# Optimization experiments

Hardware: AMD Instinct MI355X
Metric: run time of the kernel (lower is better)

## Reference

```python
import jax, jax.numpy as jnp
import numpy as np

EPS = 1e-12

def l2_normalize(x):
    # matches torch: x * rsqrt(max(sum(x^2), eps))
    ss = jnp.sum(x * x, axis=-1, keepdims=True)
    return x * jax.lax.rsqrt(jnp.maximum(ss, EPS))

B, S, D = 256, 197, 768          # batch, tokens, embed_dim (ViT-B)
H, LEN, KS, POOL = 12, 5, 17, 50  # heads, prompt length, conv kernel, pool_size
DUAL_LEN = 2 * (LEN + KS - 1)     # 42
PD = D + (KS - 1) * H             # 960


def setup_inputs() -> dict:
    key = jax.random.key(0)
    ks = jax.random.split(key, 8)
    x_embed = jax.random.normal(ks[0], (B, S, D), jnp.float32)
    # learned params
    prompt = jax.random.uniform(ks[1], (1, DUAL_LEN, PD), jnp.float32, -1.0, 1.0)
    prompt_key = jax.random.uniform(ks[2], (POOL, D // 4), jnp.float32, -1.0, 1.0)
    W1 = jax.random.normal(ks[3], (D // 2, D), jnp.float32) * (1.0 / np.sqrt(D))
    b1 = jnp.zeros((D // 2,), jnp.float32)
    W2 = jax.random.normal(ks[4], (D // 4, D // 2), jnp.float32) * (1.0 / np.sqrt(D // 2))
    b2 = jnp.zeros((D // 4,), jnp.float32)
    return {"x_embed": x_embed, "prompt": prompt, "prompt_key": prompt_key,
            "W1": W1, "b1": b1, "W2": W2, "b2": b2, "layer_num": 0}


def reference(x_embed, prompt, prompt_key, W1, b1, W2, b2, layer_num):
    # embedding_key == 'mean'
    x_mean = jnp.mean(x_embed, axis=1)                       # [B, D]
    # prompt_embed_matcher: Linear(D, D/2) -> ReLU -> Linear(D/2, D/4)
    h = jax.nn.relu(x_mean @ W1.T + b1)                      # [B, D/2]
    feat = h @ W2.T + b2                                     # [B, D/4]
    # cosine similarity against key pool (eval path: full pool)
    key_norm = l2_normalize(prompt_key)                      # [POOL, D/4]
    x_norm = l2_normalize(feat)                              # [B, D/4]
    similarity = x_norm @ key_norm.T                         # [B, POOL] == (K @ X^T)^T
    # prefix-tune prompt: repeat over batch and split into (dual, len, heads, head_dim)
    p = prompt[layer_num]                                    # [DUAL_LEN, PD]
    Ltot, E = p.shape
    batched_prompt = jnp.broadcast_to(p, (x_embed.shape[0], Ltot, E))
    batched_prompt = batched_prompt.reshape(x_embed.shape[0], 2, Ltot // 2, H, E // H)
    return similarity, x_norm, batched_prompt
```

## Files before the change

kernel.cpp:

```cpp
#include <hip/hip_runtime.h>

#define NB 256
#define NS 197
#define ND 768
#define ND2 384
#define ND4 192
#define NPOOL 50
#define PROMPT_FLOATS 40320
#define PROMPT_V4 10080
#define TB 2

__global__ __launch_bounds__(768) void k_mean_bcast(
    const float* __restrict__ x,
    const float* __restrict__ prompt,
    const int* __restrict__ layer_num,
    float* __restrict__ xmean,
    float* __restrict__ out_prompt)
{
    const int b = blockIdx.x;
    const int tid = threadIdx.x;
    const int lane = tid % 192;
    const int g = tid / 192;

    const float4* __restrict__ xr =
        reinterpret_cast<const float4*>(x) + (size_t)b * (NS * (ND / 4));
    float4 acc = make_float4(0.f, 0.f, 0.f, 0.f);
    for (int s = g; s < NS; s += 4) {
        float4 v = xr[s * (ND / 4) + lane];
        acc.x += v.x; acc.y += v.y; acc.z += v.z; acc.w += v.w;
    }
    __shared__ float4 part[4][192];
    part[g][lane] = acc;
    __syncthreads();
    if (g == 0) {
        float4 p0 = part[0][lane], p1 = part[1][lane];
        float4 p2 = part[2][lane], p3 = part[3][lane];
        const float inv = 1.0f / (float)NS;
        float4 m;
        m.x = (p0.x + p1.x + p2.x + p3.x) * inv;
        m.y = (p0.y + p1.y + p2.y + p3.y) * inv;
        m.z = (p0.z + p1.z + p2.z + p3.z) * inv;
        m.w = (p0.w + p1.w + p2.w + p3.w) * inv;
        reinterpret_cast<float4*>(xmean + (size_t)b * ND)[lane] = m;
    }

    const float4* __restrict__ pv =
        reinterpret_cast<const float4*>(prompt + (size_t)layer_num[0] * PROMPT_FLOATS);
    float4* __restrict__ ov =
        reinterpret_cast<float4*>(out_prompt) + (size_t)b * PROMPT_V4;
    for (int i = tid; i < PROMPT_V4; i += 768) {
        ov[i] = pv[i];
    }
}

__global__ __launch_bounds__(512) void k_mlp(
    const float* __restrict__ xmean,
    const float* __restrict__ W1,
    const float* __restrict__ b1,
    const float* __restrict__ W2,
    const float* __restrict__ b2,
    const float* __restrict__ key,
    float* __restrict__ sim,
    float* __restrict__ xnorm)
{
    const int tid = threadIdx.x;
    const int g   = tid >> 4;
    const int l   = tid & 15;
    const int b0  = blockIdx.x * TB;

    __shared__ __align__(16) float xm[TB][ND];
    __shared__ __align__(16) float hs[TB][ND2];
    __shared__ __align__(16) float fs[TB][ND4];
    __shared__ float rs[TB];

    {
        const float4* __restrict__ src =
            reinterpret_cast<const float4*>(xmean + (size_t)b0 * ND);
        float4* dst = reinterpret_cast<float4*>(&xm[0][0]);
        for (int i = tid; i < TB * ND / 4; i += 512) dst[i] = src[i];
    }
    __syncthreads();

    {
        const float4* __restrict__ x0v = reinterpret_cast<const float4*>(&xm[0][0]);
        const float4* __restrict__ x1v = reinterpret_cast<const float4*>(&xm[1][0]);
        for (int r = 0; r < ND2 / 32; ++r) {
            const int i = g + 32 * r;
            const float4* __restrict__ w =
                reinterpret_cast<const float4*>(W1 + (size_t)i * ND);
            float a0 = 0.f, a1 = 0.f;
            #pragma unroll
            for (int s = 0; s < ND / 64; ++s) {
                float4 wv = w[s * 16 + l];
                float4 x0 = x0v[s * 16 + l];
                float4 x1 = x1v[s * 16 + l];
                a0 += wv.x * x0.x + wv.y * x0.y + wv.z * x0.z + wv.w * x0.w;
                a1 += wv.x * x1.x + wv.y * x1.y + wv.z * x1.z + wv.w * x1.w;
            }
            #pragma unroll
            for (int m = 8; m; m >>= 1) {
                a0 += __shfl_xor(a0, m);
                a1 += __shfl_xor(a1, m);
            }
            if (l == 0) {
                float bias = b1[i];
                hs[0][i] = fmaxf(a0 + bias, 0.f);
                hs[1][i] = fmaxf(a1 + bias, 0.f);
            }
        }
    }
    __syncthreads();

    {
        const float4* __restrict__ h0v = reinterpret_cast<const float4*>(&hs[0][0]);
        const float4* __restrict__ h1v = reinterpret_cast<const float4*>(&hs[1][0]);
        for (int r = 0; r < ND4 / 32; ++r) {
            const int j = g + 32 * r;
            const float4* __restrict__ w =
                reinterpret_cast<const float4*>(W2 + (size_t)j * ND2);
            float a0 = 0.f, a1 = 0.f;
            #pragma unroll
            for (int s = 0; s < ND2 / 64; ++s) {
                float4 wv = w[s * 16 + l];
                float4 h0 = h0v[s * 16 + l];
                float4 h1 = h1v[s * 16 + l];
                a0 += wv.x * h0.x + wv.y * h0.y + wv.z * h0.z + wv.w * h0.w;
                a1 += wv.x * h1.x + wv.y * h1.y + wv.z * h1.z + wv.w * h1.w;
            }
            #pragma unroll
            for (int m = 8; m; m >>= 1) {
                a0 += __shfl_xor(a0, m);
                a1 += __shfl_xor(a1, m);
            }
            if (l == 0) {
                float bias = b2[j];
                fs[0][j] = a0 + bias;
                fs[1][j] = a1 + bias;
            }
        }
    }
    __syncthreads();

    if (tid < TB * 64) {
        const int w = tid >> 6, ll = tid & 63;
        float v0 = fs[w][ll], v1 = fs[w][ll + 64], v2 = fs[w][ll + 128];
        float ss = v0 * v0 + v1 * v1 + v2 * v2;
        #pragma unroll
        for (int m = 32; m; m >>= 1) ss += __shfl_xor(ss, m);
        if (ll == 0) rs[w] = rsqrtf(fmaxf(ss, 1e-12f));
    }
    __syncthreads();

    for (int i = tid; i < TB * ND4; i += 512) {
        const int b = i / ND4, j = i - b * ND4;
        float v = fs[b][j] * rs[b];
        fs[b][j] = v;
        xnorm[(size_t)(b0 + b) * ND4 + j] = v;
    }
    __syncthreads();

    {
        const float4* __restrict__ x0v = reinterpret_cast<const float4*>(&fs[0][0]);
        const float4* __restrict__ x1v = reinterpret_cast<const float4*>(&fs[1][0]);
        for (int p = g; p < NPOOL; p += 32) {
            const float4* __restrict__ kr =
                reinterpret_cast<const float4*>(key + (size_t)p * ND4);
            float kk = 0.f, d0 = 0.f, d1 = 0.f;
            #pragma unroll
            for (int s = 0; s < ND4 / 64; ++s) {
                float4 kv = kr[s * 16 + l];
                float4 x0 = x0v[s * 16 + l];
                float4 x1 = x1v[s * 16 + l];
                kk += kv.x * kv.x + kv.y * kv.y + kv.z * kv.z + kv.w * kv.w;
                d0 += kv.x * x0.x + kv.y * x0.y + kv.z * x0.z + kv.w * x0.w;
                d1 += kv.x * x1.x + kv.y * x1.y + kv.z * x1.z + kv.w * x1.w;
            }
            #pragma unroll
            for (int m = 8; m; m >>= 1) {
                kk += __shfl_xor(kk, m);
                d0 += __shfl_xor(d0, m);
                d1 += __shfl_xor(d1, m);
            }
            if (l == 0) {
                float krs = rsqrtf(fmaxf(kk, 1e-12f));
                sim[(size_t)(b0 + 0) * NPOOL + p] = d0 * krs;
                sim[(size_t)(b0 + 1) * NPOOL + p] = d1 * krs;
            }
        }
    }
}

extern "C" void kernel_launch(void* const* d_in, const int* in_sizes, int n_in,
                              void* d_out, int out_size, void* d_ws, size_t ws_size,
                              hipStream_t stream) {
    const float* x        = (const float*)d_in[0];
    const float* prompt   = (const float*)d_in[1];
    const float* key      = (const float*)d_in[2];
    const float* W1       = (const float*)d_in[3];
    const float* b1       = (const float*)d_in[4];
    const float* W2       = (const float*)d_in[5];
    const float* b2       = (const float*)d_in[6];
    const int*   layer_nm = (const int*)d_in[7];

    float* out        = (float*)d_out;
    float* sim        = out;
    float* xnorm      = out + 12800;
    float* out_prompt = out + 12800 + 49152;

    float* xmean = (float*)d_ws;

    hipLaunchKernelGGL(k_mean_bcast, dim3(NB), dim3(768), 0, stream,
                       x, prompt, layer_nm, xmean, out_prompt);
    hipLaunchKernelGGL(k_mlp, dim3(NB / TB), dim3(512), 0, stream,
                       xmean, W1, b1, W2, b2, key, sim, xnorm);
}
```

Baseline: 327.0 us.

## Fuse mean, MLP, similarity and prompt broadcast into one per-batch kernel

Merges the mean/broadcast kernel and the MLP/similarity kernel into a single kernel with one 768-thread block per batch row. The token mean stays in shared memory and feeds the MLP directly, so the workspace round trip and the second launch go away. In exchange, each block now streams the full W1/W2 weights for one row instead of sharing them across two rows, which doubles weight reads, though these likely hit in L2. The prompt broadcast writes are moved to the end of the block.

Result: faster. 266.1 us (-18.6%).

```diff
diff --git a/kernel.cpp b/kernel.cpp
--- a/kernel.cpp
+++ b/kernel.cpp
@@ -8,184 +8,144 @@
 #define NPOOL 50
 #define PROMPT_FLOATS 40320
 #define PROMPT_V4 10080
-#define TB 2
 
-__global__ __launch_bounds__(768) void k_mean_bcast(
+__global__ __launch_bounds__(768) void k_fused(
     const float* __restrict__ x,
     const float* __restrict__ prompt,
     const int* __restrict__ layer_num,
-    float* __restrict__ xmean,
-    float* __restrict__ out_prompt)
-{
-    const int b = blockIdx.x;
-    const int tid = threadIdx.x;
-    const int lane = tid % 192;
-    const int g = tid / 192;
-
-    const float4* __restrict__ xr =
-        reinterpret_cast<const float4*>(x) + (size_t)b * (NS * (ND / 4));
-    float4 acc = make_float4(0.f, 0.f, 0.f, 0.f);
-    for (int s = g; s < NS; s += 4) {
-        float4 v = xr[s * (ND / 4) + lane];
-        acc.x += v.x; acc.y += v.y; acc.z += v.z; acc.w += v.w;
-    }
-    __shared__ float4 part[4][192];
-    part[g][lane] = acc;
-    __syncthreads();
-    if (g == 0) {
-        float4 p0 = part[0][lane], p1 = part[1][lane];
-        float4 p2 = part[2][lane], p3 = part[3][lane];
-        const float inv = 1.0f / (float)NS;
-        float4 m;
-        m.x = (p0.x + p1.x + p2.x + p3.x) * inv;
-        m.y = (p0.y + p1.y + p2.y + p3.y) * inv;
-        m.z = (p0.z + p1.z + p2.z + p3.z) * inv;
-        m.w = (p0.w + p1.w + p2.w + p3.w) * inv;
-        reinterpret_cast<float4*>(xmean + (size_t)b * ND)[lane] = m;
-    }
-
-    const float4* __restrict__ pv =
-        reinterpret_cast<const float4*>(prompt + (size_t)layer_num[0] * PROMPT_FLOATS);
-    float4* __restrict__ ov =
-        reinterpret_cast<float4*>(out_prompt) + (size_t)b * PROMPT_V4;
-    for (int i = tid; i < PROMPT_V4; i += 768) {
-        ov[i] = pv[i];
-    }
-}
-
-__global__ __launch_bounds__(512) void k_mlp(
-    const float* __restrict__ xmean,
     const float* __restrict__ W1,
     const float* __restrict__ b1,
     const float* __restrict__ W2,
     const float* __restrict__ b2,
     const float* __restrict__ key,
     float* __restrict__ sim,
-    float* __restrict__ xnorm)
+    float* __restrict__ xnorm,
+    float* __restrict__ out_prompt)
 {
+    const int b   = blockIdx.x;
     const int tid = threadIdx.x;
     const int g   = tid >> 4;
     const int l   = tid & 15;
-    const int b0  = blockIdx.x * TB;
 
-    __shared__ __align__(16) float xm[TB][ND];
-    __shared__ __align__(16) float hs[TB][ND2];
-    __shared__ __align__(16) float fs[TB][ND4];
-    __shared__ float rs[TB];
+    __shared__ __align__(16) float4 part[4][192];
+    __shared__ __align__(16) float xm[ND];
+    __shared__ __align__(16) float hs[ND2];
+    __shared__ __align__(16) float fs[ND4];
+    __shared__ float rsv;
 
     {
-        const float4* __restrict__ src =
-            reinterpret_cast<const float4*>(xmean + (size_t)b0 * ND);
-        float4* dst = reinterpret_cast<float4*>(&xm[0][0]);
-        for (int i = tid; i < TB * ND / 4; i += 512) dst[i] = src[i];
-    }
-    __syncthreads();
-
-    {
-        const float4* __restrict__ x0v = reinterpret_cast<const float4*>(&xm[0][0]);
-        const float4* __restrict__ x1v = reinterpret_cast<const float4*>(&xm[1][0]);
-        for (int r = 0; r < ND2 / 32; ++r) {
-            const int i = g + 32 * r;
-            const float4* __restrict__ w =
-                reinterpret_cast<const float4*>(W1 + (size_t)i * ND);
-            float a0 = 0.f, a1 = 0.f;
-            #pragma unroll
-            for (int s = 0; s < ND / 64; ++s) {
-                float4 wv = w[s * 16 + l];
-                float4 x0 = x0v[s * 16 + l];
-                float4 x1 = x1v[s * 16 + l];
-                a0 += wv.x * x0.x + wv.y * x0.y + wv.z * x0.z + wv.w * x0.w;
-                a1 += wv.x * x1.x + wv.y * x1.y + wv.z * x1.z + wv.w * x1.w;
-            }
-            #pragma unroll
-            for (int m = 8; m; m >>= 1) {
-                a0 += __shfl_xor(a0, m);
-                a1 += __shfl_xor(a1, m);
-            }
-            if (l == 0) {
-                float bias = b1[i];
-                hs[0][i] = fmaxf(a0 + bias, 0.f);
-                hs[1][i] = fmaxf(a1 + bias, 0.f);
-            }
+        const int lane = tid % 192;
+        const int sg   = tid / 192;
+        const float4* __restrict__ xr =
+            reinterpret_cast<const float4*>(x) + (size_t)b * (NS * (ND / 4));
+        float4 acc = make_float4(0.f, 0.f, 0.f, 0.f);
+        for (int s = sg; s < NS; s += 4) {
+            float4 v = xr[s * (ND / 4) + lane];
+            acc.x += v.x; acc.y += v.y; acc.z += v.z; acc.w += v.w;
+        }
+        part[sg][lane] = acc;
+        __syncthreads();
+        if (sg == 0) {
+            float4 p0 = part[0][lane], p1 = part[1][lane];
+            float4 p2 = part[2][lane], p3 = part[3][lane];
+            const float inv = 1.0f / (float)NS;
+            float4 m;
+            m.x = (p0.x + p1.x + p2.x + p3.x) * inv;
+            m.y = (p0.y + p1.y + p2.y + p3.y) * inv;
+            m.z = (p0.z + p1.z + p2.z + p3.z) * inv;
+            m.w = (p0.w + p1.w + p2.w + p3.w) * inv;
+            reinterpret_cast<float4*>(xm)[lane] = m;
         }
     }
     __syncthreads();
 
     {
-        const float4* __restrict__ h0v = reinterpret_cast<const float4*>(&hs[0][0]);
-        const float4* __restrict__ h1v = reinterpret_cast<const float4*>(&hs[1][0]);
-        for (int r = 0; r < ND4 / 32; ++r) {
-            const int j = g + 32 * r;
+        const float4* __restrict__ xv = reinterpret_cast<const float4*>(xm);
+        #pragma unroll
+        for (int r = 0; r < ND2 / 48; ++r) {
+            const int i = g + 48 * r;
             const float4* __restrict__ w =
-                reinterpret_cast<const float4*>(W2 + (size_t)j * ND2);
-            float a0 = 0.f, a1 = 0.f;
+                reinterpret_cast<const float4*>(W1 + (size_t)i * ND);
+            float a = 0.f;
             #pragma unroll
-            for (int s = 0; s < ND2 / 64; ++s) {
+            for (int s = 0; s < ND / 64; ++s) {
                 float4 wv = w[s * 16 + l];
-                float4 h0 = h0v[s * 16 + l];
-                float4 h1 = h1v[s * 16 + l];
-                a0 += wv.x * h0.x + wv.y * h0.y + wv.z * h0.z + wv.w * h0.w;
-                a1 += wv.x * h1.x + wv.y * h1.y + wv.z * h1.z + wv.w * h1.w;
+                float4 xv4 = xv[s * 16 + l];
+                a += wv.x * xv4.x + wv.y * xv4.y + wv.z * xv4.z + wv.w * xv4.w;
             }
             #pragma unroll
-            for (int m = 8; m; m >>= 1) {
-                a0 += __shfl_xor(a0, m);
-                a1 += __shfl_xor(a1, m);
-            }
-            if (l == 0) {
-                float bias = b2[j];
-                fs[0][j] = a0 + bias;
-                fs[1][j] = a1 + bias;
-            }
+            for (int m = 8; m; m >>= 1) a += __shfl_xor(a, m);
+            if (l == 0) hs[i] = fmaxf(a + b1[i], 0.f);
         }
     }
     __syncthreads();
 
-    if (tid < TB * 64) {
-        const int w = tid >> 6, ll = tid & 63;
-        float v0 = fs[w][ll], v1 = fs[w][ll + 64], v2 = fs[w][ll + 128];
+    {
+        const float4* __restrict__ hv = reinterpret_cast<const float4*>(hs);
+        #pragma unroll
+        for (int r = 0; r < ND4 / 48; ++r) {
+            const int j = g + 48 * r;
+            const float4* __restrict__ w =
+                reinterpret_cast<const float4*>(W2 + (size_t)j * ND2);
+            float a = 0.f;
+            #pragma unroll
+            for (int s = 0; s < ND2 / 64; ++s) {
+                float4 wv = w[s * 16 + l];
+                float4 hv4 = hv[s * 16 + l];
+                a += wv.x * hv4.x + wv.y * hv4.y + wv.z * hv4.z + wv.w * hv4.w;
+            }
+            #pragma unroll
+            for (int m = 8; m; m >>= 1) a += __shfl_xor(a, m);
+            if (l == 0) fs[j] = a + b2[j];
+        }
+    }
+    __syncthreads();
+
+    if (tid < 64) {
+        float v0 = fs[tid], v1 = fs[tid + 64], v2 = fs[tid + 128];
         float ss = v0 * v0 + v1 * v1 + v2 * v2;
         #pragma unroll
         for (int m = 32; m; m >>= 1) ss += __shfl_xor(ss, m);
-        if (ll == 0) rs[w] = rsqrtf(fmaxf(ss, 1e-12f));
+        if (tid == 0) rsv = rsqrtf(fmaxf(ss, 1e-12f));
     }
     __syncthreads();
 
-    for (int i = tid; i < TB * ND4; i += 512) {
-        const int b = i / ND4, j = i - b * ND4;
-        float v = fs[b][j] * rs[b];
-        fs[b][j] = v;
-        xnorm[(size_t)(b0 + b) * ND4 + j] = v;
+    if (tid < ND4) {
+        float v = fs[tid] * rsv;
+        fs[tid] = v;
+        xnorm[(size_t)b * ND4 + tid] = v;
     }
     __syncthreads();
 
     {
-        const float4* __restrict__ x0v = reinterpret_cast<const float4*>(&fs[0][0]);
-        const float4* __restrict__ x1v = reinterpret_cast<const float4*>(&fs[1][0]);
-        for (int p = g; p < NPOOL; p += 32) {
+        const float4* __restrict__ xv = reinterpret_cast<const float4*>(fs);
+        for (int p = g; p < NPOOL; p += 48) {
             const float4* __restrict__ kr =
                 reinterpret_cast<const float4*>(key + (size_t)p * ND4);
-            float kk = 0.f, d0 = 0.f, d1 = 0.f;
+            float kk = 0.f, d = 0.f;
             #pragma unroll
             for (int s = 0; s < ND4 / 64; ++s) {
                 float4 kv = kr[s * 16 + l];
-                float4 x0 = x0v[s * 16 + l];
-                float4 x1 = x1v[s * 16 + l];
+                float4 xv4 = xv[s * 16 + l];
                 kk += kv.x * kv.x + kv.y * kv.y + kv.z * kv.z + kv.w * kv.w;
-                d0 += kv.x * x0.x + kv.y * x0.y + kv.z * x0.z + kv.w * x0.w;
-                d1 += kv.x * x1.x + kv.y * x1.y + kv.z * x1.z + kv.w * x1.w;
+                d  += kv.x * xv4.x + kv.y * xv4.y + kv.z * xv4.z + kv.w * xv4.w;
             }
             #pragma unroll
             for (int m = 8; m; m >>= 1) {
                 kk += __shfl_xor(kk, m);
-                d0 += __shfl_xor(d0, m);
-                d1 += __shfl_xor(d1, m);
+                d  += __shfl_xor(d, m);
             }
-            if (l == 0) {
-                float krs = rsqrtf(fmaxf(kk, 1e-12f));
-                sim[(size_t)(b0 + 0) * NPOOL + p] = d0 * krs;
-                sim[(size_t)(b0 + 1) * NPOOL + p] = d1 * krs;
-            }
+            if (l == 0) sim[(size_t)b * NPOOL + p] = d * rsqrtf(fmaxf(kk, 1e-12f));
+        }
+    }
+
+    {
+        const float4* __restrict__ pv =
+            reinterpret_cast<const float4*>(prompt + (size_t)layer_num[0] * PROMPT_FLOATS);
+        float4* __restrict__ ov =
+            reinterpret_cast<float4*>(out_prompt) + (size_t)b * PROMPT_V4;
+        for (int i = tid; i < PROMPT_V4; i += 768) {
+            ov[i] = pv[i];
         }
     }
 }
@@ -207,10 +167,7 @@
     float* xnorm      = out + 12800;
     float* out_prompt = out + 12800 + 49152;
 
-    float* xmean = (float*)d_ws;
-
-    hipLaunchKernelGGL(k_mean_bcast, dim3(NB), dim3(768), 0, stream,
-                       x, prompt, layer_nm, xmean, out_prompt);
-    hipLaunchKernelGGL(k_mlp, dim3(NB / TB), dim3(512), 0, stream,
-                       xmean, W1, b1, W2, b2, key, sim, xnorm);
+    hipLaunchKernelGGL(k_fused, dim3(NB), dim3(768), 0, stream,
+                       x, prompt, layer_nm, W1, b1, W2, b2, key,
+                       sim, xnorm, out_prompt);
 }
```

## Split token-mean into per-chunk partial sums and batch four rows per MLP block

Applied to the files above, without the earlier changes.

The mean reduction now runs as 2048 blocks, each summing a 25-row chunk of one batch element and copying a slice of the prompt broadcast. Partial sums go to workspace and are combined in the MLP kernel's prologue, which removes the shared-memory combine step. The MLP kernel now handles four batch rows per block instead of two, so each W1/W2/key load is reused across more rows. In exchange it writes more intermediate data, and the MLP stage runs on only 64 blocks.

New measurement: 281.9 us. -13.8%, faster.

```diff
diff --git a/kernel.cpp b/kernel.cpp
--- a/kernel.cpp
+++ b/kernel.cpp
@@ -3,58 +3,52 @@
 #define NB 256
 #define NS 197
 #define ND 768
+#define NDV4 192
 #define ND2 384
 #define ND4 192
 #define NPOOL 50
 #define PROMPT_FLOATS 40320
 #define PROMPT_V4 10080
-#define TB 2
-
-__global__ __launch_bounds__(768) void k_mean_bcast(
+#define SCH 8
+#define ROWS 25
+#define PSLICE 1260
+#define TB 4
+
+__global__ __launch_bounds__(192) void k_partial(
     const float* __restrict__ x,
     const float* __restrict__ prompt,
     const int* __restrict__ layer_num,
-    float* __restrict__ xmean,
+    float* __restrict__ partial,
     float* __restrict__ out_prompt)
 {
-    const int b = blockIdx.x;
-    const int tid = threadIdx.x;
-    const int lane = tid % 192;
-    const int g = tid / 192;
+    const int blk = blockIdx.x;
+    const int b = blk >> 3;
+    const int c = blk & 7;
+    const int t = threadIdx.x;
 
     const float4* __restrict__ xr =
-        reinterpret_cast<const float4*>(x) + (size_t)b * (NS * (ND / 4));
+        reinterpret_cast<const float4*>(x) + (size_t)b * (NS * NDV4);
+    const int s0 = c * ROWS;
+    const int s1 = (s0 + ROWS < NS) ? (s0 + ROWS) : NS;
     float4 acc = make_float4(0.f, 0.f, 0.f, 0.f);
-    for (int s = g; s < NS; s += 4) {
-        float4 v = xr[s * (ND / 4) + lane];
+    for (int s = s0; s < s1; ++s) {
+        float4 v = xr[(size_t)s * NDV4 + t];
         acc.x += v.x; acc.y += v.y; acc.z += v.z; acc.w += v.w;
     }
-    __shared__ float4 part[4][192];
-    part[g][lane] = acc;
-    __syncthreads();
-    if (g == 0) {
-        float4 p0 = part[0][lane], p1 = part[1][lane];
-        float4 p2 = part[2][lane], p3 = part[3][lane];
-        const float inv = 1.0f / (float)NS;
-        float4 m;
-        m.x = (p0.x + p1.x + p2.x + p3.x) * inv;
-        m.y = (p0.y + p1.y + p2.y + p3.y) * inv;
-        m.z = (p0.z + p1.z + p2.z + p3.z) * inv;
-        m.w = (p0.w + p1.w + p2.w + p3.w) * inv;
-        reinterpret_cast<float4*>(xmean + (size_t)b * ND)[lane] = m;
-    }
+    reinterpret_cast<float4*>(partial)[(size_t)blk * NDV4 + t] = acc;
 
     const float4* __restrict__ pv =
         reinterpret_cast<const float4*>(prompt + (size_t)layer_num[0] * PROMPT_FLOATS);
     float4* __restrict__ ov =
         reinterpret_cast<float4*>(out_prompt) + (size_t)b * PROMPT_V4;
-    for (int i = tid; i < PROMPT_V4; i += 768) {
-        ov[i] = pv[i];
+    const int base = c * PSLICE;
+    for (int i = t; i < PSLICE; i += 192) {
+        ov[base + i] = pv[base + i];
     }
 }
 
 __global__ __launch_bounds__(512) void k_mlp(
-    const float* __restrict__ xmean,
+    const float* __restrict__ partial,
     const float* __restrict__ W1,
     const float* __restrict__ b1,
     const float* __restrict__ W2,
@@ -73,39 +67,58 @@
     __shared__ __align__(16) float fs[TB][ND4];
     __shared__ float rs[TB];
 
-    {
-        const float4* __restrict__ src =
-            reinterpret_cast<const float4*>(xmean + (size_t)b0 * ND);
-        float4* dst = reinterpret_cast<float4*>(&xm[0][0]);
-        for (int i = tid; i < TB * ND / 4; i += 512) dst[i] = src[i];
+    const float inv = 1.0f / (float)NS;
+    for (int idx = tid; idx < TB * NDV4; idx += 512) {
+        const int b = idx / NDV4, col = idx % NDV4;
+        const float4* __restrict__ pr =
+            reinterpret_cast<const float4*>(partial) +
+            ((size_t)(b0 + b) * SCH) * NDV4 + col;
+        float4 s = make_float4(0.f, 0.f, 0.f, 0.f);
+        #pragma unroll
+        for (int c = 0; c < SCH; ++c) {
+            float4 v = pr[(size_t)c * NDV4];
+            s.x += v.x; s.y += v.y; s.z += v.z; s.w += v.w;
+        }
+        reinterpret_cast<float4*>(&xm[b][0])[col] =
+            make_float4(s.x * inv, s.y * inv, s.z * inv, s.w * inv);
     }
     __syncthreads();
 
     {
         const float4* __restrict__ x0v = reinterpret_cast<const float4*>(&xm[0][0]);
         const float4* __restrict__ x1v = reinterpret_cast<const float4*>(&xm[1][0]);
+        const float4* __restrict__ x2v = reinterpret_cast<const float4*>(&xm[2][0]);
+        const float4* __restrict__ x3v = reinterpret_cast<const float4*>(&xm[3][0]);
         for (int r = 0; r < ND2 / 32; ++r) {
             const int i = g + 32 * r;
             const float4* __restrict__ w =
                 reinterpret_cast<const float4*>(W1 + (size_t)i * ND);
-            float a0 = 0.f, a1 = 0.f;
+            float a0 = 0.f, a1 = 0.f, a2 = 0.f, a3 = 0.f;
             #pragma unroll
             for (int s = 0; s < ND / 64; ++s) {
                 float4 wv = w[s * 16 + l];
                 float4 x0 = x0v[s * 16 + l];
                 float4 x1 = x1v[s * 16 + l];
+                float4 x2 = x2v[s * 16 + l];
+                float4 x3 = x3v[s * 16 + l];
                 a0 += wv.x * x0.x + wv.y * x0.y + wv.z * x0.z + wv.w * x0.w;
                 a1 += wv.x * x1.x + wv.y * x1.y + wv.z * x1.z + wv.w * x1.w;
+                a2 += wv.x * x2.x + wv.y * x2.y + wv.z * x2.z + wv.w * x2.w;
+                a3 += wv.x * x3.x + wv.y * x3.y + wv.z * x3.z + wv.w * x3.w;
             }
             #pragma unroll
             for (int m = 8; m; m >>= 1) {
                 a0 += __shfl_xor(a0, m);
                 a1 += __shfl_xor(a1, m);
+                a2 += __shfl_xor(a2, m);
+                a3 += __shfl_xor(a3, m);
             }
             if (l == 0) {
-                float bias = b1[i];
+                const float bias = b1[i];
                 hs[0][i] = fmaxf(a0 + bias, 0.f);
                 hs[1][i] = fmaxf(a1 + bias, 0.f);
+                hs[2][i] = fmaxf(a2 + bias, 0.f);
+                hs[3][i] = fmaxf(a3 + bias, 0.f);
             }
         }
     }
@@ -114,28 +127,38 @@
     {
         const float4* __restrict__ h0v = reinterpret_cast<const float4*>(&hs[0][0]);
         const float4* __restrict__ h1v = reinterpret_cast<const float4*>(&hs[1][0]);
+        const float4* __restrict__ h2v = reinterpret_cast<const float4*>(&hs[2][0]);
+        const float4* __restrict__ h3v = reinterpret_cast<const float4*>(&hs[3][0]);
         for (int r = 0; r < ND4 / 32; ++r) {
             const int j = g + 32 * r;
             const float4* __restrict__ w =
                 reinterpret_cast<const float4*>(W2 + (size_t)j * ND2);
-            float a0 = 0.f, a1 = 0.f;
+            float a0 = 0.f, a1 = 0.f, a2 = 0.f, a3 = 0.f;
             #pragma unroll
             for (int s = 0; s < ND2 / 64; ++s) {
                 float4 wv = w[s * 16 + l];
                 float4 h0 = h0v[s * 16 + l];
                 float4 h1 = h1v[s * 16 + l];
+                float4 h2 = h2v[s * 16 + l];
+                float4 h3 = h3v[s * 16 + l];
                 a0 += wv.x * h0.x + wv.y * h0.y + wv.z * h0.z + wv.w * h0.w;
                 a1 += wv.x * h1.x + wv.y * h1.y + wv.z * h1.z + wv.w * h1.w;
+                a2 += wv.x * h2.x + wv.y * h2.y + wv.z * h2.z + wv.w * h2.w;
+                a3 += wv.x * h3.x + wv.y * h3.y + wv.z * h3.z + wv.w * h3.w;
             }
             #pragma unroll
             for (int m = 8; m; m >>= 1) {
                 a0 += __shfl_xor(a0, m);
                 a1 += __shfl_xor(a1, m);
+                a2 += __shfl_xor(a2, m);
+                a3 += __shfl_xor(a3, m);
             }
             if (l == 0) {
-                float bias = b2[j];
+                const float bias = b2[j];
                 fs[0][j] = a0 + bias;
                 fs[1][j] = a1 + bias;
+                fs[2][j] = a2 + bias;
+                fs[3][j] = a3 + bias;
             }
         }
     }
@@ -151,8 +174,8 @@
     }
     __syncthreads();
 
-    for (int i = tid; i < TB * ND4; i += 512) {
-        const int b = i / ND4, j = i - b * ND4;
+    for (int idx = tid; idx < TB * ND4; idx += 512) {
+        const int b = idx / ND4, j = idx - b * ND4;
         float v = fs[b][j] * rs[b];
         fs[b][j] = v;
         xnorm[(size_t)(b0 + b) * ND4 + j] = v;
@@ -162,29 +185,39 @@
     {
         const float4* __restrict__ x0v = reinterpret_cast<const float4*>(&fs[0][0]);
         const float4* __restrict__ x1v = reinterpret_cast<const float4*>(&fs[1][0]);
+        const float4* __restrict__ x2v = reinterpret_cast<const float4*>(&fs[2][0]);
+        const float4* __restrict__ x3v = reinterpret_cast<const float4*>(&fs[3][0]);
         for (int p = g; p < NPOOL; p += 32) {
             const float4* __restrict__ kr =
                 reinterpret_cast<const float4*>(key + (size_t)p * ND4);
-            float kk = 0.f, d0 = 0.f, d1 = 0.f;
+            float kk = 0.f, d0 = 0.f, d1 = 0.f, d2 = 0.f, d3 = 0.f;
             #pragma unroll
             for (int s = 0; s < ND4 / 64; ++s) {
                 float4 kv = kr[s * 16 + l];
                 float4 x0 = x0v[s * 16 + l];
                 float4 x1 = x1v[s * 16 + l];
+                float4 x2 = x2v[s * 16 + l];
+                float4 x3 = x3v[s * 16 + l];
                 kk += kv.x * kv.x + kv.y * kv.y + kv.z * kv.z + kv.w * kv.w;
                 d0 += kv.x * x0.x + kv.y * x0.y + kv.z * x0.z + kv.w * x0.w;
                 d1 += kv.x * x1.x + kv.y * x1.y + kv.z * x1.z + kv.w * x1.w;
+                d2 += kv.x * x2.x + kv.y * x2.y + kv.z * x2.z + kv.w * x2.w;
+                d3 += kv.x * x3.x + kv.y * x3.y + kv.z * x3.z + kv.w * x3.w;
             }
             #pragma unroll
             for (int m = 8; m; m >>= 1) {
                 kk += __shfl_xor(kk, m);
                 d0 += __shfl_xor(d0, m);
                 d1 += __shfl_xor(d1, m);
+                d2 += __shfl_xor(d2, m);
+                d3 += __shfl_xor(d3, m);
             }
             if (l == 0) {
-                float krs = rsqrtf(fmaxf(kk, 1e-12f));
+                const float krs = rsqrtf(fmaxf(kk, 1e-12f));
                 sim[(size_t)(b0 + 0) * NPOOL + p] = d0 * krs;
                 sim[(size_t)(b0 + 1) * NPOOL + p] = d1 * krs;
+                sim[(size_t)(b0 + 2) * NPOOL + p] = d2 * krs;
+                sim[(size_t)(b0 + 3) * NPOOL + p] = d3 * krs;
             }
         }
     }
@@ -207,10 +240,10 @@
     float* xnorm      = out + 12800;
     float* out_prompt = out + 12800 + 49152;
 
-    float* xmean = (float*)d_ws;
-
-    hipLaunchKernelGGL(k_mean_bcast, dim3(NB), dim3(768), 0, stream,
-                       x, prompt, layer_nm, xmean, out_prompt);
+    float* partial = (float*)d_ws;
+
+    hipLaunchKernelGGL(k_partial, dim3(NB * SCH), dim3(192), 0, stream,
+                       x, prompt, layer_nm, partial, out_prompt);
     hipLaunchKernelGGL(k_mlp, dim3(NB / TB), dim3(512), 0, stream,
-                       xmean, W1, b1, W2, b2, key, sim, xnorm);
+                       partial, W1, b1, W2, b2, key, sim, xnorm);
 }
```
